# Performance work log

Hardware: AMD Instinct MI355X
Metric: run time of the kernel (lower is better)

## Reference

```python
import jax, jax.numpy as jnp
import numpy as np

QUEST_DIM = 768
C, X, Y = 2048, 19, 19
B = 64

def setup_inputs() -> dict:
    key = jax.random.key(0)
    k1, k2, k3, k4 = jax.random.split(key, 4)
    text_fts = jax.random.normal(k1, (B, QUEST_DIM), dtype=jnp.float32)
    img_fts = jax.random.normal(k2, (B, C, X, Y), dtype=jnp.float32)
    # Linear params (PyTorch nn.Linear: y = x @ W.T + b)
    bound = 1.0 / np.sqrt(QUEST_DIM)
    W = jax.random.uniform(k3, (C, QUEST_DIM), minval=-bound, maxval=bound, dtype=jnp.float32)
    b = jax.random.uniform(k4, (C,), minval=-bound, maxval=bound, dtype=jnp.float32)
    return {"text_fts": text_fts, "img_fts": img_fts, "W": W, "b": b}

def reference(text_fts, img_fts, W, b):
    batch = text_fts.shape[0]
    q = text_fts @ W.T + b                      # [B, C]
    img_flat = img_fts.reshape(batch, C, X * Y) # [B, C, S]
    sims = jnp.einsum('bc,bcs->bs', q, img_flat)  # dot over channel dim
    weights = jax.nn.softmax(sims, axis=1)        # softmax over spatial locations
    final_ans = jnp.einsum('bcs,bs->bc', img_flat, weights)  # weighted pooling
    return final_ans
```

## Files before the change

### kernel.cpp

```cpp
#include <hip/hip_runtime.h>
#include <math.h>

#define Bsz  64
#define Cch  2048
#define Kdim 768
#define Ssp  361

__global__ __launch_bounds__(256) void k_qgemm(
    const float* __restrict__ text, const float* __restrict__ W,
    const float* __restrict__ bias, float* __restrict__ qT)
{
    const int lane = threadIdx.x & 63;
    const int wv   = threadIdx.x >> 6;
    const int c0   = blockIdx.x * 8 + wv * 2;
    const int b0   = blockIdx.y * 8;

    const float4* wA = (const float4*)(W + (size_t)c0 * Kdim);
    const float4* wB = (const float4*)(W + (size_t)(c0 + 1) * Kdim);
    const float4 a0 = wA[lane*3+0], a1 = wA[lane*3+1], a2 = wA[lane*3+2];
    const float4 g0 = wB[lane*3+0], g1 = wB[lane*3+1], g2 = wB[lane*3+2];
    const float biasA = bias[c0], biasB = bias[c0 + 1];

    for (int b = b0; b < b0 + 8; b += 2) {
        const float4* tp = (const float4*)(text + (size_t)b * Kdim);
        const float4* up = (const float4*)(text + (size_t)(b + 1) * Kdim);
        const float4 t0 = tp[lane*3+0], t1 = tp[lane*3+1], t2 = tp[lane*3+2];
        const float4 u0 = up[lane*3+0], u1 = up[lane*3+1], u2 = up[lane*3+2];

        float r00 = a0.x*t0.x + a0.y*t0.y + a0.z*t0.z + a0.w*t0.w
                  + a1.x*t1.x + a1.y*t1.y + a1.z*t1.z + a1.w*t1.w
                  + a2.x*t2.x + a2.y*t2.y + a2.z*t2.z + a2.w*t2.w;
        float r10 = g0.x*t0.x + g0.y*t0.y + g0.z*t0.z + g0.w*t0.w
                  + g1.x*t1.x + g1.y*t1.y + g1.z*t1.z + g1.w*t1.w
                  + g2.x*t2.x + g2.y*t2.y + g2.z*t2.z + g2.w*t2.w;
        float r01 = a0.x*u0.x + a0.y*u0.y + a0.z*u0.z + a0.w*u0.w
                  + a1.x*u1.x + a1.y*u1.y + a1.z*u1.z + a1.w*u1.w
                  + a2.x*u2.x + a2.y*u2.y + a2.z*u2.z + a2.w*u2.w;
        float r11 = g0.x*u0.x + g0.y*u0.y + g0.z*u0.z + g0.w*u0.w
                  + g1.x*u1.x + g1.y*u1.y + g1.z*u1.z + g1.w*u1.w
                  + g2.x*u2.x + g2.y*u2.y + g2.z*u2.z + g2.w*u2.w;
        #pragma unroll
        for (int off = 32; off; off >>= 1) {
            r00 += __shfl_xor(r00, off);
            r10 += __shfl_xor(r10, off);
            r01 += __shfl_xor(r01, off);
            r11 += __shfl_xor(r11, off);
        }
        if (lane == 0) {
            qT[(size_t)c0 * Bsz + b]           = r00 + biasA;
            qT[(size_t)(c0 + 1) * Bsz + b]     = r10 + biasB;
            qT[(size_t)c0 * Bsz + b + 1]       = r01 + biasA;
            qT[(size_t)(c0 + 1) * Bsz + b + 1] = r11 + biasB;
        }
    }
}

__global__ __launch_bounds__(384) void k_sims(
    const float* __restrict__ img, const float* __restrict__ qT,
    float* __restrict__ sims_part)
{
    const int b  = blockIdx.x;
    const int cg = blockIdx.y;
    const int tid = threadIdx.x;

    __shared__ float qL[16];
    if (tid < 16) qL[tid] = qT[(size_t)(cg * 16 + tid) * Bsz + b];
    __syncthreads();

    if (tid < Ssp) {
        const float* base = img + ((size_t)b * Cch + (size_t)cg * 16) * Ssp + tid;
        const float v0  = base[0 * Ssp],  v1  = base[1 * Ssp];
        const float v2  = base[2 * Ssp],  v3  = base[3 * Ssp];
        const float v4  = base[4 * Ssp],  v5  = base[5 * Ssp];
        const float v6  = base[6 * Ssp],  v7  = base[7 * Ssp];
        const float v8  = base[8 * Ssp],  v9  = base[9 * Ssp];
        const float v10 = base[10 * Ssp], v11 = base[11 * Ssp];
        const float v12 = base[12 * Ssp], v13 = base[13 * Ssp];
        const float v14 = base[14 * Ssp], v15 = base[15 * Ssp];
        float acc = qL[0]*v0   + qL[1]*v1   + qL[2]*v2   + qL[3]*v3
                  + qL[4]*v4   + qL[5]*v5   + qL[6]*v6   + qL[7]*v7
                  + qL[8]*v8   + qL[9]*v9   + qL[10]*v10 + qL[11]*v11
                  + qL[12]*v12 + qL[13]*v13 + qL[14]*v14 + qL[15]*v15;
        sims_part[((size_t)b * 128 + cg) * Ssp + tid] = acc;
    }
}

__global__ __launch_bounds__(384) void k_wts(
    const float* __restrict__ sims_part, float* __restrict__ wts)
{
    const int b   = blockIdx.x;
    const int tid = threadIdx.x;
    const int lane = tid & 63;
    const int wv   = tid >> 6;

    __shared__ float red[6];

    float s0 = -1e30f;
    if (tid < Ssp) {
        const float* sp = sims_part + (size_t)b * 128 * Ssp + tid;
        float a = 0.f;
        for (int g0 = 0; g0 < 128; g0 += 16) {
            float v[16];
            #pragma unroll
            for (int j = 0; j < 16; j++) v[j] = sp[(size_t)(g0 + j) * Ssp];
            #pragma unroll
            for (int j = 0; j < 16; j++) a += v[j];
        }
        s0 = a;
    }

    float m = s0;
    #pragma unroll
    for (int off = 32; off; off >>= 1) m = fmaxf(m, __shfl_xor(m, off));
    if (lane == 0) red[wv] = m;
    __syncthreads();
    m = red[0];
    #pragma unroll
    for (int w = 1; w < 6; w++) m = fmaxf(m, red[w]);
    __syncthreads();

    const float e0 = (tid < Ssp) ? __expf(s0 - m) : 0.f;
    float l = e0;
    #pragma unroll
    for (int off = 32; off; off >>= 1) l += __shfl_xor(l, off);
    if (lane == 0) red[wv] = l;
    __syncthreads();
    l = red[0] + red[1] + red[2] + red[3] + red[4] + red[5];

    if (tid < Ssp)
        wts[(size_t)b * Ssp + tid] = e0 / l;
}

__global__ __launch_bounds__(256) void k_pool(
    const float* __restrict__ img, const float* __restrict__ wts,
    float* __restrict__ out)
{
    const int b   = blockIdx.x;
    const int cg  = blockIdx.y;
    const int tid = threadIdx.x;
    const int lane = tid & 63;
    const int wv   = tid >> 6;

    __shared__ float outL[128];

    const float* wb = wts + (size_t)b * Ssp;
    const float w0 = wb[lane];
    const float w1 = wb[lane + 64];
    const float w2 = wb[lane + 128];
    const float w3 = wb[lane + 192];
    const float w4 = wb[lane + 256];
    const float w5 = (lane + 320 < Ssp) ? wb[lane + 320] : 0.f;

    const int cbase = cg * 128 + wv * 32;
    for (int cc = 0; cc < 32; cc += 4) {
        const float* p0 = img + ((size_t)b * Cch + cbase + cc) * Ssp;
        const float* p1 = p0 + Ssp;
        const float* p2 = p1 + Ssp;
        const float* p3 = p2 + Ssp;
        float r0, r1, r2, r3;
        {
            float v00=p0[lane],     v01=p0[lane+64],  v02=p0[lane+128],
                  v03=p0[lane+192], v04=p0[lane+256];
            float v10=p1[lane],     v11=p1[lane+64],  v12=p1[lane+128],
                  v13=p1[lane+192], v14=p1[lane+256];
            float v20=p2[lane],     v21=p2[lane+64],  v22=p2[lane+128],
                  v23=p2[lane+192], v24=p2[lane+256];
            float v30=p3[lane],     v31=p3[lane+64],  v32=p3[lane+128],
                  v33=p3[lane+192], v34=p3[lane+256];
            float v05 = 0.f, v15 = 0.f, v25 = 0.f, v35 = 0.f;
            if (lane + 320 < Ssp) {
                v05 = p0[lane+320]; v15 = p1[lane+320];
                v25 = p2[lane+320]; v35 = p3[lane+320];
            }
            r0 = v00*w0 + v01*w1 + v02*w2 + v03*w3 + v04*w4 + v05*w5;
            r1 = v10*w0 + v11*w1 + v12*w2 + v13*w3 + v14*w4 + v15*w5;
            r2 = v20*w0 + v21*w1 + v22*w2 + v23*w3 + v24*w4 + v25*w5;
            r3 = v30*w0 + v31*w1 + v32*w2 + v33*w3 + v34*w4 + v35*w5;
        }
        #pragma unroll
        for (int off = 32; off; off >>= 1) {
            r0 += __shfl_xor(r0, off);
            r1 += __shfl_xor(r1, off);
            r2 += __shfl_xor(r2, off);
            r3 += __shfl_xor(r3, off);
        }
        if (lane == 0) {
            outL[wv * 32 + cc]     = r0;
            outL[wv * 32 + cc + 1] = r1;
            outL[wv * 32 + cc + 2] = r2;
            outL[wv * 32 + cc + 3] = r3;
        }
    }
    __syncthreads();
    if (tid < 128)
        out[(size_t)b * Cch + cg * 128 + tid] = outL[tid];
}

extern "C" void kernel_launch(void* const* d_in, const int* in_sizes, int n_in,
                              void* d_out, int out_size, void* d_ws, size_t ws_size,
                              hipStream_t stream) {
    const float* text = (const float*)d_in[0];
    const float* img  = (const float*)d_in[1];
    const float* W    = (const float*)d_in[2];
    const float* bias = (const float*)d_in[3];
    float* out = (float*)d_out;

    float* qT        = (float*)d_ws;
    float* sims_part = qT + (size_t)Cch * Bsz;
    float* wts       = sims_part + (size_t)Bsz * 128 * Ssp;

    k_qgemm<<<dim3(256, 8),   256, 0, stream>>>(text, W, bias, qT);
    k_sims <<<dim3(Bsz, 128), 384, 0, stream>>>(img, qT, sims_part);
    k_wts  <<<dim3(Bsz),      384, 0, stream>>>(sims_part, wts);
    k_pool <<<dim3(Bsz, 16),  256, 0, stream>>>(img, wts, out);
}
```

Measured before the change: 318.8 us.

## Stage image slices into LDS via global_load_lds DMA in sims and pool

```diff
diff --git a/kernel.cpp b/kernel.cpp
--- a/kernel.cpp
+++ b/kernel.cpp
@@ -5,6 +5,26 @@
 #define Cch  2048
 #define Kdim 768
 #define Ssp  361
+#define CPB  16
+#define REGF (CPB * Ssp)
+#define NFULL 22
+#define NTAIL 36
+
+__device__ __forceinline__ void dma16(const float* g, float* l) {
+    __builtin_amdgcn_global_load_lds(
+        (const __attribute__((address_space(1))) void*)(g),
+        (__attribute__((address_space(3))) void*)(l),
+        16, 0, 0);
+}
+
+__device__ __forceinline__ void stage_slice(const float* region, float* lds,
+                                            int wv, int lane) {
+    for (int i = wv; i < NFULL + 1; i += 6) {
+        if (i < NFULL || lane < NTAIL)
+            dma16(region + i * 256 + lane * 4, lds + i * 256);
+    }
+    asm volatile("s_waitcnt vmcnt(0)" ::: "memory");
+}
 
 __global__ __launch_bounds__(256) void k_qgemm(
     const float* __restrict__ text, const float* __restrict__ W,
@@ -62,25 +82,23 @@
     const int b  = blockIdx.x;
     const int cg = blockIdx.y;
     const int tid = threadIdx.x;
-
-    __shared__ float qL[16];
-    if (tid < 16) qL[tid] = qT[(size_t)(cg * 16 + tid) * Bsz + b];
+    const int lane = tid & 63;
+    const int wv   = tid >> 6;
+
+    __shared__ float lds[REGF];
+    __shared__ float qL[CPB];
+
+    if (tid < CPB) qL[tid] = qT[(size_t)(cg * CPB + tid) * Bsz + b];
+
+    const float* region = img + ((size_t)b * Cch + (size_t)cg * CPB) * Ssp;
+    stage_slice(region, lds, wv, lane);
     __syncthreads();
 
     if (tid < Ssp) {
-        const float* base = img + ((size_t)b * Cch + (size_t)cg * 16) * Ssp + tid;
-        const float v0  = base[0 * Ssp],  v1  = base[1 * Ssp];
-        const float v2  = base[2 * Ssp],  v3  = base[3 * Ssp];
-        const float v4  = base[4 * Ssp],  v5  = base[5 * Ssp];
-        const float v6  = base[6 * Ssp],  v7  = base[7 * Ssp];
-        const float v8  = base[8 * Ssp],  v9  = base[9 * Ssp];
-        const float v10 = base[10 * Ssp], v11 = base[11 * Ssp];
-        const float v12 = base[12 * Ssp], v13 = base[13 * Ssp];
-        const float v14 = base[14 * Ssp], v15 = base[15 * Ssp];
-        float acc = qL[0]*v0   + qL[1]*v1   + qL[2]*v2   + qL[3]*v3
-                  + qL[4]*v4   + qL[5]*v5   + qL[6]*v6   + qL[7]*v7
-                  + qL[8]*v8   + qL[9]*v9   + qL[10]*v10 + qL[11]*v11
-                  + qL[12]*v12 + qL[13]*v13 + qL[14]*v14 + qL[15]*v15;
+        float acc = 0.f;
+        #pragma unroll
+        for (int c = 0; c < CPB; c++)
+            acc += qL[c] * lds[c * Ssp + tid];
         sims_part[((size_t)b * 128 + cg) * Ssp + tid] = acc;
     }
 }
@@ -131,7 +149,7 @@
         wts[(size_t)b * Ssp + tid] = e0 / l;
 }
 
-__global__ __launch_bounds__(256) void k_pool(
+__global__ __launch_bounds__(384) void k_pool(
     const float* __restrict__ img, const float* __restrict__ wts,
     float* __restrict__ out)
 {
@@ -141,59 +159,36 @@
     const int lane = tid & 63;
     const int wv   = tid >> 6;
 
-    __shared__ float outL[128];
-
-    const float* wb = wts + (size_t)b * Ssp;
-    const float w0 = wb[lane];
-    const float w1 = wb[lane + 64];
-    const float w2 = wb[lane + 128];
-    const float w3 = wb[lane + 192];
-    const float w4 = wb[lane + 256];
-    const float w5 = (lane + 320 < Ssp) ? wb[lane + 320] : 0.f;
-
-    const int cbase = cg * 128 + wv * 32;
-    for (int cc = 0; cc < 32; cc += 4) {
-        const float* p0 = img + ((size_t)b * Cch + cbase + cc) * Ssp;
-        const float* p1 = p0 + Ssp;
-        const float* p2 = p1 + Ssp;
-        const float* p3 = p2 + Ssp;
-        float r0, r1, r2, r3;
-        {
-            float v00=p0[lane],     v01=p0[lane+64],  v02=p0[lane+128],
-                  v03=p0[lane+192], v04=p0[lane+256];
-            float v10=p1[lane],     v11=p1[lane+64],  v12=p1[lane+128],
-                  v13=p1[lane+192], v14=p1[lane+256];
-            float v20=p2[lane],     v21=p2[lane+64],  v22=p2[lane+128],
-                  v23=p2[lane+192], v24=p2[lane+256];
-            float v30=p3[lane],     v31=p3[lane+64],  v32=p3[lane+128],
-                  v33=p3[lane+192], v34=p3[lane+256];
-            float v05 = 0.f, v15 = 0.f, v25 = 0.f, v35 = 0.f;
-            if (lane + 320 < Ssp) {
-                v05 = p0[lane+320]; v15 = p1[lane+320];
-                v25 = p2[lane+320]; v35 = p3[lane+320];
-            }
-            r0 = v00*w0 + v01*w1 + v02*w2 + v03*w3 + v04*w4 + v05*w5;
-            r1 = v10*w0 + v11*w1 + v12*w2 + v13*w3 + v14*w4 + v15*w5;
-            r2 = v20*w0 + v21*w1 + v22*w2 + v23*w3 + v24*w4 + v25*w5;
-            r3 = v30*w0 + v31*w1 + v32*w2 + v33*w3 + v34*w4 + v35*w5;
-        }
+    __shared__ float lds[REGF];
+    __shared__ float wL[Ssp];
+    __shared__ float partial[6 * CPB];
+
+    if (tid < Ssp) wL[tid] = wts[(size_t)b * Ssp + tid];
+
+    const float* region = img + ((size_t)b * Cch + (size_t)cg * CPB) * Ssp;
+    stage_slice(region, lds, wv, lane);
+    __syncthreads();
+
+    const int c    = lane & 15;
+    const int sl   = lane >> 4;
+    const int s_lo = sl * 90 + (sl > 0 ? 1 : 0);
+    const int s_hi = s_lo + (sl > 0 ? 90 : 91);
+
+    float p = 0.f;
+    for (int s = s_lo + wv; s < s_hi; s += 6)
+        p += lds[c * Ssp + s] * wL[s];
+
+    p += __shfl_xor(p, 16);
+    p += __shfl_xor(p, 32);
+    if (lane < CPB) partial[wv * CPB + lane] = p;
+    __syncthreads();
+
+    if (tid < CPB) {
+        float r = partial[tid];
         #pragma unroll
-        for (int off = 32; off; off >>= 1) {
-            r0 += __shfl_xor(r0, off);
-            r1 += __shfl_xor(r1, off);
-            r2 += __shfl_xor(r2, off);
-            r3 += __shfl_xor(r3, off);
-        }
-        if (lane == 0) {
-            outL[wv * 32 + cc]     = r0;
-            outL[wv * 32 + cc + 1] = r1;
-            outL[wv * 32 + cc + 2] = r2;
-            outL[wv * 32 + cc + 3] = r3;
-        }
-    }
-    __syncthreads();
-    if (tid < 128)
-        out[(size_t)b * Cch + cg * 128 + tid] = outL[tid];
+        for (int w = 1; w < 6; w++) r += partial[w * CPB + tid];
+        out[(size_t)b * Cch + (size_t)cg * CPB + tid] = r;
+    }
 }
 
 extern "C" void kernel_launch(void* const* d_in, const int* in_sizes, int n_in,
@@ -212,5 +207,5 @@
     k_qgemm<<<dim3(256, 8),   256, 0, stream>>>(text, W, bias, qT);
     k_sims <<<dim3(Bsz, 128), 384, 0, stream>>>(img, qT, sims_part);
     k_wts  <<<dim3(Bsz),      384, 0, stream>>>(sims_part, wts);
-    k_pool <<<dim3(Bsz, 16),  256, 0, stream>>>(img, wts, out);
-}
+    k_pool <<<dim3(Bsz, 128), 384, 0, stream>>>(img, wts, out);
+}
```

Result: no change. 316.5 us (-0.7%).
